# Performance work log

Hardware: AMD Instinct MI355X
Metric: run time of the kernel (lower is better)

The kernel has to match this reference:

```python
import jax, jax.numpy as jnp
import numpy as np
from jax import lax

D_MODEL = 1024
D_STATE = 16
D_CONV = 4
EXPAND = 2
D_INNER = D_MODEL * EXPAND
B, T = 2, 1024


def setup_inputs() -> dict:
    key = jax.random.key(0)
    ks = jax.random.split(key, 8)
    s = 0.02
    x = jax.random.normal(ks[0], (B, T, D_MODEL), dtype=jnp.float32)
    in_proj_w = jax.random.normal(ks[1], (D_MODEL, 2 * D_INNER), dtype=jnp.float32) * s
    conv_w = jax.random.normal(ks[2], (D_INNER, 1, D_CONV), dtype=jnp.float32) * s  # depthwise [O, I/G=1, K]
    conv_b = jax.random.normal(ks[3], (D_INNER,), dtype=jnp.float32) * s
    x_proj_w = jax.random.normal(ks[4], (D_INNER, 2 * D_STATE + 1), dtype=jnp.float32) * s
    dt_proj_w = jax.random.normal(ks[5], (1, D_INNER), dtype=jnp.float32) * s
    dt_proj_b = jax.random.normal(ks[6], (D_INNER,), dtype=jnp.float32) * s
    # Canonical Mamba init: A_log = log(1..d_state) broadcast over d_inner
    A_log = jnp.broadcast_to(jnp.log(jnp.arange(1, D_STATE + 1, dtype=jnp.float32))[None, :], (D_INNER, D_STATE))
    D_param = jnp.ones((D_INNER,), dtype=jnp.float32)
    c_proj_w = jax.random.normal(ks[7], (D_INNER, D_MODEL), dtype=jnp.float32) * s
    return {"x": x, "in_proj_w": in_proj_w, "conv_w": conv_w, "conv_b": conv_b,
            "x_proj_w": x_proj_w, "dt_proj_w": dt_proj_w, "dt_proj_b": dt_proj_b,
            "A_log": A_log, "D_param": D_param, "c_proj_w": c_proj_w}


def _mamba_fwd(x, in_proj_w, conv_w, conv_b, x_proj_w, dt_proj_w, dt_proj_b, A_log, D_param, c_proj_w):
    Bb, Tt, _ = x.shape
    xz = jnp.einsum('btd,de->bte', x, in_proj_w)          # [B,T,2*Di]
    x_branch, z = jnp.split(xz, 2, axis=-1)               # [B,T,Di] each
    # Causal depthwise conv1d: pad left K-1 (== torch pad both + slice[:T])
    xb = jnp.transpose(x_branch, (0, 2, 1))               # [B,Di,T]
    xb = lax.conv_general_dilated(xb, conv_w, window_strides=(1,),
                                  padding=[(D_CONV - 1, 0)],
                                  feature_group_count=D_INNER,
                                  dimension_numbers=('NCH', 'OIH', 'NCH'))
    xb = xb + conv_b[None, :, None]
    x_branch = jax.nn.silu(jnp.transpose(xb, (0, 2, 1)))  # [B,T,Di]
    x_ssm = jnp.einsum('btd,dk->btk', x_branch, x_proj_w) # [B,T,2S+1]
    B_t = x_ssm[:, :, :D_STATE]                            # [B,T,S]
    C_t = x_ssm[:, :, D_STATE:2 * D_STATE]                 # [B,T,S]
    dt = x_ssm[:, :, -1:]                                  # [B,T,1]
    dt = jax.nn.softplus(jnp.einsum('btk,kd->btd', dt, dt_proj_w) + dt_proj_b)  # [B,T,Di]
    A = -jnp.exp(A_log)                                    # [Di,S]
    A_bar = jnp.exp(dt[..., None] * A[None, None])         # [B,T,Di,S]
    Bx = (dt[..., None] * B_t[:, :, None, :]) * x_branch[..., None]  # [B,T,Di,S]

    def step(h, inp):
        a, bx, c = inp                                     # [B,Di,S],[B,Di,S],[B,S]
        h = a * h + bx
        y = jnp.einsum('bds,bs->bd', h, c)
        return h, y

    h0 = jnp.zeros((Bb, D_INNER, D_STATE), dtype=x.dtype)
    _, ys = lax.scan(step, h0,
                     (jnp.transpose(A_bar, (1, 0, 2, 3)),
                      jnp.transpose(Bx, (1, 0, 2, 3)),
                      jnp.transpose(C_t, (1, 0, 2))))
    y = jnp.transpose(ys, (1, 0, 2))                       # [B,T,Di]
    y = y + D_param[None, None, :] * x_branch
    y = y * jax.nn.silu(z)
    return jnp.einsum('btd,de->bte', y, c_proj_w)          # [B,T,d_model]


def reference(x, in_proj_w, conv_w, conv_b, x_proj_w, dt_proj_w, dt_proj_b, A_log, D_param, c_proj_w):
    return _mamba_fwd(x, in_proj_w, conv_w, conv_b, x_proj_w, dt_proj_w, dt_proj_b, A_log, D_param, c_proj_w)
```

## Files before the change

### kernel.cpp

```cpp
#include <hip/hip_runtime.h>
#include <math.h>

#define DMODEL 1024
#define DSTATE 16
#define DCONV 4
#define DINNER 2048
#define BATCH 2
#define SEQ 1024
#define BT (BATCH*SEQ)
#define NC 32
#define LC 32

typedef unsigned short ushort_t;
typedef __attribute__((ext_vector_type(8))) short short8;
typedef __attribute__((ext_vector_type(4))) float f32x4;

__device__ __forceinline__ ushort_t f2bf(float f) {
    union { float f; unsigned int u; } v; v.f = f;
    unsigned int r = v.u + 0x7fffu + ((v.u >> 16) & 1u);
    return (ushort_t)(r >> 16);
}
__device__ __forceinline__ float bf2f(ushort_t u) {
    union { unsigned int u; float f; } v; v.u = ((unsigned int)u) << 16;
    return v.f;
}
__device__ __forceinline__ float softplusf(float x) {
    return (x > 20.f) ? x : log1pf(__expf(x));
}

#define GLOAD_LDS16(G, L) \
  __builtin_amdgcn_global_load_lds((const __attribute__((address_space(1))) void*)(G), \
                                   (__attribute__((address_space(3))) void*)(L), 16, 0, 0)

__global__ __launch_bounds__(256) void prep_kernel(const float* __restrict__ x,
                                                   ushort_t* __restrict__ xbf,
                                                   const float* __restrict__ w1,
                                                   ushort_t* __restrict__ w1T,
                                                   const float* __restrict__ w2,
                                                   ushort_t* __restrict__ w2T,
                                                   float* __restrict__ zacc)
{
    __shared__ float t[32][33];
    const int bid = blockIdx.x;
    const int tid = threadIdx.x;

    if (bid < 1024) {
        size_t i = ((size_t)bid * 256 + tid) * 8;
        float4 a = *(const float4*)&x[i];
        float4 b = *(const float4*)&x[i + 4];
        uint4 p;
        p.x = (unsigned)f2bf(a.x) | ((unsigned)f2bf(a.y) << 16);
        p.y = (unsigned)f2bf(a.z) | ((unsigned)f2bf(a.w) << 16);
        p.z = (unsigned)f2bf(b.x) | ((unsigned)f2bf(b.y) << 16);
        p.w = (unsigned)f2bf(b.z) | ((unsigned)f2bf(b.w) << 16);
        *(uint4*)&xbf[i] = p;
        if (bid < 66) {
            size_t z = ((size_t)bid * 256 + tid) * 4;
            *(float4*)&zacc[z] = make_float4(0.f, 0.f, 0.f, 0.f);
        }
        return;
    }

    const float* in; ushort_t* out; int R, Cc, r0, c0;
    if (bid < 5120) {
        int b2 = bid - 1024;
        in = w1; out = w1T; R = DMODEL; Cc = 2 * DINNER;
        r0 = (b2 >> 7) * 32; c0 = (b2 & 127) * 32;
    } else {
        int b3 = bid - 5120;
        in = w2; out = w2T; R = DINNER; Cc = DMODEL;
        r0 = (b3 >> 5) * 32; c0 = (b3 & 31) * 32;
    }
    {
        int lr = tid >> 3, lc4 = (tid & 7) * 4;
        float4 v = *(const float4*)&in[(size_t)(r0 + lr) * Cc + c0 + lc4];
        t[lr][lc4 + 0] = v.x; t[lr][lc4 + 1] = v.y;
        t[lr][lc4 + 2] = v.z; t[lr][lc4 + 3] = v.w;
    }
    __syncthreads();
    {
        int oc = tid >> 3, rq = (tid & 7) * 4;
        ushort4 u;
        u.x = f2bf(t[rq + 0][oc]);
        u.y = f2bf(t[rq + 1][oc]);
        u.z = f2bf(t[rq + 2][oc]);
        u.w = f2bf(t[rq + 3][oc]);
        *(ushort4*)&out[(size_t)(c0 + oc) * R + r0 + rq] = u;
    }
}

__global__ __launch_bounds__(256) void gemm_in(const ushort_t* __restrict__ A,
                                               const ushort_t* __restrict__ Bt,
                                               float* __restrict__ xzx,
                                               ushort_t* __restrict__ zsil)
{
    constexpr int BM = 128, BN = 128, BK = 64;
    constexpr int AL = BM * BK / (256 * 8);
    constexpr int BL = BN * BK / (256 * 8);
    constexpr int FM = BM / 32;
    constexpr int FN = BN / 32;
    const int K = DMODEL;
    __shared__ __align__(16) ushort_t Al[BM * BK];
    __shared__ __align__(16) ushort_t Bl[BN * BK];

    const int tid  = threadIdx.x;
    const int lane = tid & 63;
    const int wid  = tid >> 6;
    const int wr   = wid >> 1;
    const int wc   = wid & 1;
    const int bm   = blockIdx.y * BM;
    const int bn   = blockIdx.x * BN;

    f32x4 acc[FM][FN] = {};

    for (int k0 = 0; k0 < K; k0 += BK) {
#pragma unroll
        for (int j = 0; j < AL; j++) {
            int chunk = j * 256 + tid;
            GLOAD_LDS16(&A[(size_t)(bm + (chunk >> 3)) * K + k0 + (chunk & 7) * 8],
                        &Al[(size_t)(j * 256 + wid * 64) * 8]);
        }
#pragma unroll
        for (int j = 0; j < BL; j++) {
            int chunk = j * 256 + tid;
            GLOAD_LDS16(&Bt[(size_t)(bn + (chunk >> 3)) * K + k0 + (chunk & 7) * 8],
                        &Bl[(size_t)(j * 256 + wid * 64) * 8]);
        }
        __syncthreads();

#pragma unroll
        for (int kk = 0; kk < 2; kk++) {
            short8 af[FM], bf[FN];
#pragma unroll
            for (int m = 0; m < FM; m++)
                af[m] = *(const short8*)&Al[(wr * (BM / 2) + m * 16 + (lane & 15)) * BK
                                            + (lane >> 4) * 8 + kk * 32];
#pragma unroll
            for (int n = 0; n < FN; n++)
                bf[n] = *(const short8*)&Bl[(wc * (BN / 2) + n * 16 + (lane & 15)) * BK
                                            + (lane >> 4) * 8 + kk * 32];
#pragma unroll
            for (int m = 0; m < FM; m++)
#pragma unroll
                for (int n = 0; n < FN; n++)
                    acc[m][n] = __builtin_amdgcn_mfma_f32_16x16x32_bf16(af[m], bf[n], acc[m][n], 0, 0, 0);
        }
        __syncthreads();
    }

    if (bn < DINNER) {
#pragma unroll
        for (int m = 0; m < FM; m++)
#pragma unroll
            for (int n = 0; n < FN; n++) {
                int row0 = bm + wr * (BM / 2) + m * 16 + (lane >> 4) * 4;
                int col  = bn + wc * (BN / 2) + n * 16 + (lane & 15);
#pragma unroll
                for (int r = 0; r < 4; r++)
                    xzx[(size_t)(row0 + r) * DINNER + col] = acc[m][n][r];
            }
    } else {
#pragma unroll
        for (int m = 0; m < FM; m++)
#pragma unroll
            for (int n = 0; n < FN; n++) {
                int row0 = bm + wr * (BM / 2) + m * 16 + (lane >> 4) * 4;
                int col  = bn - DINNER + wc * (BN / 2) + n * 16 + (lane & 15);
#pragma unroll
                for (int r = 0; r < 4; r++) {
                    float z = acc[m][n][r];
                    zsil[(size_t)(row0 + r) * DINNER + col] = f2bf(z / (1.f + __expf(-z)));
                }
            }
    }
}

template<int BM, int BN>
__global__ __launch_bounds__(256) void gemm_bt(const ushort_t* __restrict__ A,
                                               const ushort_t* __restrict__ Bt,
                                               float* __restrict__ C,
                                               int M, int N, int K)
{
    constexpr int BK = 64;
    constexpr int AL = BM * BK / (256 * 8);
    constexpr int BL = BN * BK / (256 * 8);
    constexpr int FM = BM / 32;
    constexpr int FN = BN / 32;
    __shared__ __align__(16) ushort_t Al[BM * BK];
    __shared__ __align__(16) ushort_t Bl[BN * BK];

    const int tid  = threadIdx.x;
    const int lane = tid & 63;
    const int wid  = tid >> 6;
    const int wr   = wid >> 1;
    const int wc   = wid & 1;
    const int bm   = blockIdx.y * BM;
    const int bn   = blockIdx.x * BN;

    f32x4 acc[FM][FN] = {};

    for (int k0 = 0; k0 < K; k0 += BK) {
#pragma unroll
        for (int j = 0; j < AL; j++) {
            int chunk = j * 256 + tid;
            GLOAD_LDS16(&A[(size_t)(bm + (chunk >> 3)) * K + k0 + (chunk & 7) * 8],
                        &Al[(size_t)(j * 256 + wid * 64) * 8]);
        }
#pragma unroll
        for (int j = 0; j < BL; j++) {
            int chunk = j * 256 + tid;
            GLOAD_LDS16(&Bt[(size_t)(bn + (chunk >> 3)) * K + k0 + (chunk & 7) * 8],
                        &Bl[(size_t)(j * 256 + wid * 64) * 8]);
        }
        __syncthreads();

#pragma unroll
        for (int kk = 0; kk < 2; kk++) {
            short8 af[FM], bf[FN];
#pragma unroll
            for (int m = 0; m < FM; m++)
                af[m] = *(const short8*)&Al[(wr * (BM / 2) + m * 16 + (lane & 15)) * BK
                                            + (lane >> 4) * 8 + kk * 32];
#pragma unroll
            for (int n = 0; n < FN; n++)
                bf[n] = *(const short8*)&Bl[(wc * (BN / 2) + n * 16 + (lane & 15)) * BK
                                            + (lane >> 4) * 8 + kk * 32];
#pragma unroll
            for (int m = 0; m < FM; m++)
#pragma unroll
                for (int n = 0; n < FN; n++)
                    acc[m][n] = __builtin_amdgcn_mfma_f32_16x16x32_bf16(af[m], bf[n], acc[m][n], 0, 0, 0);
        }
        __syncthreads();
    }

#pragma unroll
    for (int m = 0; m < FM; m++)
#pragma unroll
        for (int n = 0; n < FN; n++) {
            int row0 = bm + wr * (BM / 2) + m * 16 + (lane >> 4) * 4;
            int col  = bn + wc * (BN / 2) + n * 16 + (lane & 15);
#pragma unroll
            for (int r = 0; r < 4; r++)
                C[(size_t)(row0 + r) * N + col] = acc[m][n][r];
        }
}

__global__ __launch_bounds__(256) void conv_silu_kernel(const float* __restrict__ xzx,
                                                        const float* __restrict__ cw,
                                                        const float* __restrict__ cb,
                                                        float* __restrict__ xb_rm)
{
    __shared__ float tile[64 + 3][64];
    const int b  = blockIdx.z;
    const int t0 = blockIdx.x * 64;
    const int d0 = blockIdx.y * 64;
    const int tid = threadIdx.x;

    for (int e = tid; e < 67 * 16; e += 256) {
        int r  = e / 16;
        int c4 = (e % 16) * 4;
        int t  = t0 - 3 + r;
        float4 v = make_float4(0.f, 0.f, 0.f, 0.f);
        if (t >= 0)
            v = *(const float4*)&xzx[((size_t)b * SEQ + t) * DINNER + d0 + c4];
        *(float4*)&tile[r][c4] = v;
    }
    __syncthreads();

    const int dl = tid & 63;
    const int tb = tid >> 6;
    const int d  = d0 + dl;
    const float w0 = cw[d * 4 + 0], w1 = cw[d * 4 + 1];
    const float w2 = cw[d * 4 + 2], w3 = cw[d * 4 + 3];
    const float bias = cb[d];

#pragma unroll
    for (int ii = 0; ii < 16; ii++) {
        int tl = tb + 4 * ii;
        float s = bias;
        s = fmaf(tile[tl + 0][dl], w0, s);
        s = fmaf(tile[tl + 1][dl], w1, s);
        s = fmaf(tile[tl + 2][dl], w2, s);
        s = fmaf(tile[tl + 3][dl], w3, s);
        float sil = s / (1.f + __expf(-s));
        xb_rm[((size_t)b * SEQ + t0 + tl) * DINNER + d] = sil;
    }
}

__global__ __launch_bounds__(256) void xproj_kernel(const float* __restrict__ xb,
                                                    const float* __restrict__ w,
                                                    float* __restrict__ Btb,
                                                    float* __restrict__ Ctb,
                                                    float* __restrict__ dtraw)
{
    __shared__ float xs[8][256];
    __shared__ float ws[256][33];
    const int bt0 = blockIdx.x * 8;
    const int kc  = blockIdx.y * 256;
    const int tid = threadIdx.x;
    const int r = tid >> 5, n = tid & 31;

#pragma unroll
    for (int j = 0; j < 2; j++) {
        int e4 = (j * 256 + tid) * 4;
        int rr = e4 >> 8, cc = e4 & 255;
        *(float4*)&xs[rr][cc] = *(const float4*)&xb[(size_t)(bt0 + rr) * DINNER + kc + cc];
    }
    {
        const float* wsrc = w + (size_t)kc * 33;
        float* wdst = &ws[0][0];
        for (int e4 = tid; e4 < 2112; e4 += 256)
            *(float4*)&wdst[e4 * 4] = *(const float4*)&wsrc[e4 * 4];
    }
    __syncthreads();

    float acc = 0.f;
#pragma unroll 16
    for (int kk = 0; kk < 256; kk += 4) {
        float4 xv = *(const float4*)&xs[r][kk];
        acc = fmaf(xv.x, ws[kk + 0][n], acc);
        acc = fmaf(xv.y, ws[kk + 1][n], acc);
        acc = fmaf(xv.z, ws[kk + 2][n], acc);
        acc = fmaf(xv.w, ws[kk + 3][n], acc);
    }
    float dacc = 0.f;
#pragma unroll
    for (int j = 0; j < 8; j++)
        dacc = fmaf(xs[r][n * 8 + j], ws[n * 8 + j][32], dacc);
#pragma unroll
    for (int off = 16; off; off >>= 1)
        dacc += __shfl_xor(dacc, off, 32);

    if (n < 16) atomicAdd(&Btb[(bt0 + r) * 16 + n], acc);
    else        atomicAdd(&Ctb[(bt0 + r) * 16 + (n - 16)], acc);
    if (n == 0) atomicAdd(&dtraw[bt0 + r], dacc);
}

__device__ __forceinline__ void qpowers(float q, float* a)
{
    float q2 = q * q, q4 = q2 * q2, q8 = q4 * q4;
    a[0] = q;        a[1] = q2;       a[2] = q2 * q;   a[3] = q4;
    a[4] = q4 * q;   a[5] = q4 * q2;  a[6] = q4 * a[2];a[7] = q8;
    a[8] = q8 * q;   a[9] = q8 * q2;  a[10]= q8 * a[2];a[11]= q8 * q4;
    a[12]= q8 * a[4];a[13]= q8 * a[5];a[14]= q8 * a[6];a[15]= q8 * q8;
}

__device__ __forceinline__ bool a_structure_ok(const float* A_log, int d, float As2_0)
{
    bool ok = true;
#pragma unroll
    for (int s = 1; s < 16; s++) {
        float v = -__expf(A_log[d * 16 + s]) * 1.44269504f;
        ok &= (fabsf(v - (float)(s + 1) * As2_0) <= 1e-4f * (float)(s + 1) * fabsf(As2_0));
    }
    return ok;
}

__global__ __launch_bounds__(256) void scan1_kernel(const float* __restrict__ xb,
                                                    const float* __restrict__ dtraw,
                                                    const float* __restrict__ Btb,
                                                    const float* __restrict__ A_log,
                                                    const float* __restrict__ dtw,
                                                    const float* __restrict__ dtb,
                                                    float* __restrict__ Hend,
                                                    float* __restrict__ dtsum)
{
    __shared__ float raw[LC];
    __shared__ float xs[LC][256];
    __shared__ float Bs[LC][16];

    const int tid = threadIdx.x;
    const int c   = blockIdx.x;
    const int b   = blockIdx.z;
    const int d0  = blockIdx.y * 256;
    const int d   = d0 + tid;
    const int t0  = c * LC;

    if (tid < LC / 4)
        *(float4*)&raw[tid * 4] = *(const float4*)&dtraw[b * SEQ + t0 + tid * 4];
    if (tid < 128)
        *(float4*)&Bs[0][tid * 4] = *(const float4*)&Btb[((size_t)b * SEQ + t0) * 16 + tid * 4];
#pragma unroll
    for (int j = 0; j < 8; j++) {
        int e = j * 256 + tid;
        int rr = e >> 6, c4 = (e & 63) * 4;
        *(float4*)&xs[rr][c4] = *(const float4*)&xb[((size_t)b * SEQ + t0 + rr) * DINNER + d0 + c4];
    }

    const float wd = dtw[d], bd = dtb[d];
    const float As2_0 = -__expf(A_log[d * 16]) * 1.44269504f;
    const bool fast = a_structure_ok(A_log, d, As2_0);

    float h[16];
#pragma unroll
    for (int s = 0; s < 16; s++) h[s] = 0.f;
    float dsum = 0.f;
    __syncthreads();

    if (fast) {
#pragma unroll 2
        for (int t = 0; t < LC; t++) {
            float dt = softplusf(fmaf(raw[t], wd, bd));
            float xv = xs[t][tid];
            float Bv[16];
#pragma unroll
            for (int s4 = 0; s4 < 4; s4++)
                *(float4*)&Bv[s4 * 4] = *(const float4*)&Bs[t][s4 * 4];
            float a[16];
            qpowers(exp2f(dt * As2_0), a);
            float dtx = dt * xv;
            dsum += dt;
#pragma unroll
            for (int s = 0; s < 16; s++)
                h[s] = fmaf(a[s], h[s], Bv[s] * dtx);
        }
    } else {
        float As2[16];
#pragma unroll
        for (int s = 0; s < 16; s++)
            As2[s] = -__expf(A_log[d * 16 + s]) * 1.44269504f;
#pragma unroll 2
        for (int t = 0; t < LC; t++) {
            float dt = softplusf(fmaf(raw[t], wd, bd));
            float xv = xs[t][tid];
            float Bv[16];
#pragma unroll
            for (int s4 = 0; s4 < 4; s4++)
                *(float4*)&Bv[s4 * 4] = *(const float4*)&Bs[t][s4 * 4];
            float dtx = dt * xv;
            dsum += dt;
#pragma unroll
            for (int s = 0; s < 16; s++)
                h[s] = fmaf(exp2f(dt * As2[s]), h[s], Bv[s] * dtx);
        }
    }

    size_t hb = (((size_t)b * NC + c) * DINNER + d) * 16;
#pragma unroll
    for (int s4 = 0; s4 < 4; s4++)
        *(float4*)&Hend[hb + s4 * 4] = *(float4*)&h[s4 * 4];
    dtsum[((size_t)b * NC + c) * DINNER + d] = dsum;
}

__global__ __launch_bounds__(256) void carry_kernel(const float* __restrict__ Hend,
                                                    const float* __restrict__ dtsum,
                                                    const float* __restrict__ A_log,
                                                    float* __restrict__ Hstart)
{
    const int idx = blockIdx.x * 256 + threadIdx.x;
    const int s = idx & 15;
    const int d = (idx >> 4) & (DINNER - 1);
    const int b = idx >> 15;
    const float As2 = -__expf(A_log[d * 16 + s]) * 1.44269504f;
    float hs = 0.f;
    for (int c = 0; c < NC; c++) {
        size_t off = ((size_t)b * NC + c);
        float P  = exp2f(As2 * dtsum[off * DINNER + d]);
        size_t hi = (off * DINNER + d) * 16 + s;
        float he = Hend[hi];
        Hstart[hi] = hs;
        hs = fmaf(P, hs, he);
    }
}

__global__ __launch_bounds__(256) void scan3_kernel(const float* __restrict__ xb,
                                                    const float* __restrict__ dtraw,
                                                    const float* __restrict__ Btb,
                                                    const float* __restrict__ Ctb,
                                                    const float* __restrict__ A_log,
                                                    const float* __restrict__ dtw,
                                                    const float* __restrict__ dtb,
                                                    const float* __restrict__ Hstart,
                                                    const ushort_t* __restrict__ zsil,
                                                    const float* __restrict__ Dp,
                                                    ushort_t* __restrict__ ygb)
{
    __shared__ float raw[LC];
    __shared__ float xs[LC][256];
    __shared__ float Bs[LC][16];
    __shared__ float Cs[LC][16];

    const int tid = threadIdx.x;
    const int c   = blockIdx.x;
    const int b   = blockIdx.z;
    const int d0  = blockIdx.y * 256;
    const int d   = d0 + tid;
    const int t0  = c * LC;

    if (tid < LC / 4)
        *(float4*)&raw[tid * 4] = *(const float4*)&dtraw[b * SEQ + t0 + tid * 4];
    if (tid < 128)
        *(float4*)&Bs[0][tid * 4] = *(const float4*)&Btb[((size_t)b * SEQ + t0) * 16 + tid * 4];
    else {
        int u = tid - 128;
        *(float4*)&Cs[0][u * 4] = *(const float4*)&Ctb[((size_t)b * SEQ + t0) * 16 + u * 4];
    }
#pragma unroll
    for (int j = 0; j < 8; j++) {
        int e = j * 256 + tid;
        int rr = e >> 6, c4 = (e & 63) * 4;
        *(float4*)&xs[rr][c4] = *(const float4*)&xb[((size_t)b * SEQ + t0 + rr) * DINNER + d0 + c4];
    }

    const float wd = dtw[d], bd = dtb[d];
    const float Dd = Dp[d];
    const float As2_0 = -__expf(A_log[d * 16]) * 1.44269504f;
    const bool fast = a_structure_ok(A_log, d, As2_0);

    float h[16];
    {
        size_t hb = (((size_t)b * NC + c) * DINNER + d) * 16;
#pragma unroll
        for (int s4 = 0; s4 < 4; s4++)
            *(float4*)&h[s4 * 4] = *(const float4*)&Hstart[hb + s4 * 4];
    }
    __syncthreads();

    if (fast) {
#pragma unroll 2
        for (int t = 0; t < LC; t++) {
            float dt = softplusf(fmaf(raw[t], wd, bd));
            float xv = xs[t][tid];
            float Bv[16], Cv[16];
#pragma unroll
            for (int s4 = 0; s4 < 4; s4++) {
                *(float4*)&Bv[s4 * 4] = *(const float4*)&Bs[t][s4 * 4];
                *(float4*)&Cv[s4 * 4] = *(const float4*)&Cs[t][s4 * 4];
            }
            float a[16];
            qpowers(exp2f(dt * As2_0), a);
            float dtx = dt * xv;
            float acc = 0.f;
#pragma unroll
            for (int s = 0; s < 16; s++) {
                h[s] = fmaf(a[s], h[s], Bv[s] * dtx);
                acc = fmaf(h[s], Cv[s], acc);
            }
            xs[t][tid] = fmaf(Dd, xv, acc);
        }
    } else {
        float As2[16];
#pragma unroll
        for (int s = 0; s < 16; s++)
            As2[s] = -__expf(A_log[d * 16 + s]) * 1.44269504f;
#pragma unroll 2
        for (int t = 0; t < LC; t++) {
            float dt = softplusf(fmaf(raw[t], wd, bd));
            float xv = xs[t][tid];
            float Bv[16], Cv[16];
#pragma unroll
            for (int s4 = 0; s4 < 4; s4++) {
                *(float4*)&Bv[s4 * 4] = *(const float4*)&Bs[t][s4 * 4];
                *(float4*)&Cv[s4 * 4] = *(const float4*)&Cs[t][s4 * 4];
            }
            float dtx = dt * xv;
            float acc = 0.f;
#pragma unroll
            for (int s = 0; s < 16; s++) {
                h[s] = fmaf(exp2f(dt * As2[s]), h[s], Bv[s] * dtx);
                acc = fmaf(h[s], Cv[s], acc);
            }
            xs[t][tid] = fmaf(Dd, xv, acc);
        }
    }
    __syncthreads();

#pragma unroll
    for (int j = 0; j < 8; j++) {
        int e = j * 256 + tid;
        int rr = e >> 6, c4 = (e & 63) * 4;
        float4 yv = *(const float4*)&xs[rr][c4];
        ushort4 zv = *(const ushort4*)&zsil[((size_t)b * SEQ + t0 + rr) * DINNER + d0 + c4];
        ushort4 u;
        u.x = f2bf(yv.x * bf2f(zv.x));
        u.y = f2bf(yv.y * bf2f(zv.y));
        u.z = f2bf(yv.z * bf2f(zv.z));
        u.w = f2bf(yv.w * bf2f(zv.w));
        *(ushort4*)&ygb[((size_t)b * SEQ + t0 + rr) * DINNER + d0 + c4] = u;
    }
}

extern "C" void kernel_launch(void* const* d_in, const int* in_sizes, int n_in,
                              void* d_out, int out_size, void* d_ws, size_t ws_size,
                              hipStream_t stream)
{
    const float* x         = (const float*)d_in[0];
    const float* in_proj_w = (const float*)d_in[1];
    const float* conv_w    = (const float*)d_in[2];
    const float* conv_b    = (const float*)d_in[3];
    const float* x_proj_w  = (const float*)d_in[4];
    const float* dt_proj_w = (const float*)d_in[5];
    const float* dt_proj_b = (const float*)d_in[6];
    const float* A_log     = (const float*)d_in[7];
    const float* D_param   = (const float*)d_in[8];
    const float* c_proj_w  = (const float*)d_in[9];
    float* out = (float*)d_out;

    float* ws    = (float*)d_ws;
    float* xzx   = ws;
    float* xb    = xzx + (size_t)BT * DINNER;
    float* Btb   = xb  + (size_t)BT * DINNER;
    float* Ctb   = Btb + (size_t)BT * 16;
    float* dtraw = Ctb + (size_t)BT * 16;
    float* Hend  = dtraw + BT;
    float* Hstart= Hend + (size_t)BATCH * NC * DINNER * 16;
    float* dtsum = Hstart + (size_t)BATCH * NC * DINNER * 16;
    ushort_t* xbf  = (ushort_t*)(dtsum + (size_t)BATCH * NC * DINNER);
    ushort_t* w1T  = xbf + (size_t)BT * DMODEL;
    ushort_t* w2T  = w1T + (size_t)(2 * DINNER) * DMODEL;
    ushort_t* ygb  = w2T + (size_t)DMODEL * DINNER;
    ushort_t* zsil = ygb + (size_t)BT * DINNER;

    prep_kernel<<<dim3(1024 + 4096 + 2048), 256, 0, stream>>>(
        x, xbf, in_proj_w, w1T, c_proj_w, w2T, Btb);

    gemm_in<<<dim3((2 * DINNER) / 128, BT / 128), 256, 0, stream>>>(
        xbf, w1T, xzx, zsil);

    conv_silu_kernel<<<dim3(SEQ / 64, DINNER / 64, BATCH), 256, 0, stream>>>(
        xzx, conv_w, conv_b, xb);

    xproj_kernel<<<dim3(BT / 8, 8), 256, 0, stream>>>(xb, x_proj_w, Btb, Ctb, dtraw);

    scan1_kernel<<<dim3(NC, DINNER / 256, BATCH), 256, 0, stream>>>(
        xb, dtraw, Btb, A_log, dt_proj_w, dt_proj_b, Hend, dtsum);
    carry_kernel<<<dim3(BATCH * DINNER * 16 / 256), 256, 0, stream>>>(
        Hend, dtsum, A_log, Hstart);
    scan3_kernel<<<dim3(NC, DINNER / 256, BATCH), 256, 0, stream>>>(
        xb, dtraw, Btb, Ctb, A_log, dt_proj_w, dt_proj_b, Hstart, zsil, D_param, ygb);

    gemm_bt<64, 64><<<dim3(DMODEL / 64, BT / 64), 256, 0, stream>>>(
        ygb, w2T, out, BT, DMODEL, DINNER);
}
```

Measured before the change: 156.7 us.

## Store conv output in bf16 and fold chunk carry into scan3

The conv+SiLU output is now written as bf16 and read back as bf16 by xproj, scan1 and scan3, halving the traffic for that activation. The separate carry kernel is removed. Each scan3 block instead recomputes its starting state by folding the chunk-end states of all earlier chunks, using the power structure of A on the fast path. This drops one launch and the Hstart buffer, but adds redundant O(c) serial work per block (up to 31 chunk loads of 16 floats each) and a precision loss on the x branch.

```diff
diff --git a/kernel.cpp b/kernel.cpp
--- a/kernel.cpp
+++ b/kernel.cpp
@@ -249,7 +249,7 @@
 __global__ __launch_bounds__(256) void conv_silu_kernel(const float* __restrict__ xzx,
                                                         const float* __restrict__ cw,
                                                         const float* __restrict__ cb,
-                                                        float* __restrict__ xb_rm)
+                                                        ushort_t* __restrict__ xbb)
 {
     __shared__ float tile[64 + 3][64];
     const int b  = blockIdx.z;
@@ -284,11 +284,11 @@
         s = fmaf(tile[tl + 2][dl], w2, s);
         s = fmaf(tile[tl + 3][dl], w3, s);
         float sil = s / (1.f + __expf(-s));
-        xb_rm[((size_t)b * SEQ + t0 + tl) * DINNER + d] = sil;
-    }
-}
-
-__global__ __launch_bounds__(256) void xproj_kernel(const float* __restrict__ xb,
+        xbb[((size_t)b * SEQ + t0 + tl) * DINNER + d] = f2bf(sil);
+    }
+}
+
+__global__ __launch_bounds__(256) void xproj_kernel(const ushort_t* __restrict__ xbb,
                                                     const float* __restrict__ w,
                                                     float* __restrict__ Btb,
                                                     float* __restrict__ Ctb,
@@ -301,11 +301,12 @@
     const int tid = threadIdx.x;
     const int r = tid >> 5, n = tid & 31;
 
-#pragma unroll
-    for (int j = 0; j < 2; j++) {
-        int e4 = (j * 256 + tid) * 4;
-        int rr = e4 >> 8, cc = e4 & 255;
-        *(float4*)&xs[rr][cc] = *(const float4*)&xb[(size_t)(bt0 + rr) * DINNER + kc + cc];
+    {
+        int rr = tid >> 5, cc8 = (tid & 31) * 8;
+        short8 v = *(const short8*)&xbb[(size_t)(bt0 + rr) * DINNER + kc + cc8];
+#pragma unroll
+        for (int k = 0; k < 8; k++)
+            xs[rr][cc8 + k] = bf2f((ushort_t)v[k]);
     }
     {
         const float* wsrc = w + (size_t)kc * 33;
@@ -357,7 +358,22 @@
     return ok;
 }
 
-__global__ __launch_bounds__(256) void scan1_kernel(const float* __restrict__ xb,
+__device__ __forceinline__ void stage_xs(const ushort_t* __restrict__ xbb,
+                                         float (*xs)[256],
+                                         int b, int t0, int d0, int tid)
+{
+#pragma unroll
+    for (int j = 0; j < 4; j++) {
+        int e = j * 256 + tid;
+        int rr = e >> 5, cc8 = (e & 31) * 8;
+        short8 v = *(const short8*)&xbb[((size_t)b * SEQ + t0 + rr) * DINNER + d0 + cc8];
+#pragma unroll
+        for (int k = 0; k < 8; k++)
+            xs[rr][cc8 + k] = bf2f((ushort_t)v[k]);
+    }
+}
+
+__global__ __launch_bounds__(256) void scan1_kernel(const ushort_t* __restrict__ xbb,
                                                     const float* __restrict__ dtraw,
                                                     const float* __restrict__ Btb,
                                                     const float* __restrict__ A_log,
@@ -381,12 +397,7 @@
         *(float4*)&raw[tid * 4] = *(const float4*)&dtraw[b * SEQ + t0 + tid * 4];
     if (tid < 128)
         *(float4*)&Bs[0][tid * 4] = *(const float4*)&Btb[((size_t)b * SEQ + t0) * 16 + tid * 4];
-#pragma unroll
-    for (int j = 0; j < 8; j++) {
-        int e = j * 256 + tid;
-        int rr = e >> 6, c4 = (e & 63) * 4;
-        *(float4*)&xs[rr][c4] = *(const float4*)&xb[((size_t)b * SEQ + t0 + rr) * DINNER + d0 + c4];
-    }
+    stage_xs(xbb, xs, b, t0, d0, tid);
 
     const float wd = dtw[d], bd = dtb[d];
     const float As2_0 = -__expf(A_log[d * 16]) * 1.44269504f;
@@ -443,35 +454,15 @@
     dtsum[((size_t)b * NC + c) * DINNER + d] = dsum;
 }
 
-__global__ __launch_bounds__(256) void carry_kernel(const float* __restrict__ Hend,
-                                                    const float* __restrict__ dtsum,
-                                                    const float* __restrict__ A_log,
-                                                    float* __restrict__ Hstart)
-{
-    const int idx = blockIdx.x * 256 + threadIdx.x;
-    const int s = idx & 15;
-    const int d = (idx >> 4) & (DINNER - 1);
-    const int b = idx >> 15;
-    const float As2 = -__expf(A_log[d * 16 + s]) * 1.44269504f;
-    float hs = 0.f;
-    for (int c = 0; c < NC; c++) {
-        size_t off = ((size_t)b * NC + c);
-        float P  = exp2f(As2 * dtsum[off * DINNER + d]);
-        size_t hi = (off * DINNER + d) * 16 + s;
-        float he = Hend[hi];
-        Hstart[hi] = hs;
-        hs = fmaf(P, hs, he);
-    }
-}
-
-__global__ __launch_bounds__(256) void scan3_kernel(const float* __restrict__ xb,
+__global__ __launch_bounds__(256) void scan3_kernel(const ushort_t* __restrict__ xbb,
                                                     const float* __restrict__ dtraw,
                                                     const float* __restrict__ Btb,
                                                     const float* __restrict__ Ctb,
                                                     const float* __restrict__ A_log,
                                                     const float* __restrict__ dtw,
                                                     const float* __restrict__ dtb,
-                                                    const float* __restrict__ Hstart,
+                                                    const float* __restrict__ Hend,
+                                                    const float* __restrict__ dtsum,
                                                     const ushort_t* __restrict__ zsil,
                                                     const float* __restrict__ Dp,
                                                     ushort_t* __restrict__ ygb)
@@ -496,12 +487,7 @@
         int u = tid - 128;
         *(float4*)&Cs[0][u * 4] = *(const float4*)&Ctb[((size_t)b * SEQ + t0) * 16 + u * 4];
     }
-#pragma unroll
-    for (int j = 0; j < 8; j++) {
-        int e = j * 256 + tid;
-        int rr = e >> 6, c4 = (e & 63) * 4;
-        *(float4*)&xs[rr][c4] = *(const float4*)&xb[((size_t)b * SEQ + t0 + rr) * DINNER + d0 + c4];
-    }
+    stage_xs(xbb, xs, b, t0, d0, tid);
 
     const float wd = dtw[d], bd = dtb[d];
     const float Dd = Dp[d];
@@ -509,11 +495,40 @@
     const bool fast = a_structure_ok(A_log, d, As2_0);
 
     float h[16];
-    {
-        size_t hb = (((size_t)b * NC + c) * DINNER + d) * 16;
-#pragma unroll
-        for (int s4 = 0; s4 < 4; s4++)
-            *(float4*)&h[s4 * 4] = *(const float4*)&Hstart[hb + s4 * 4];
+#pragma unroll
+    for (int s = 0; s < 16; s++) h[s] = 0.f;
+
+    if (fast) {
+        for (int cc = 0; cc < c; cc++) {
+            size_t off = (size_t)b * NC + cc;
+            float P[16];
+            qpowers(exp2f(As2_0 * dtsum[off * DINNER + d]), P);
+            size_t hi = (off * DINNER + d) * 16;
+            float He[16];
+#pragma unroll
+            for (int s4 = 0; s4 < 4; s4++)
+                *(float4*)&He[s4 * 4] = *(const float4*)&Hend[hi + s4 * 4];
+#pragma unroll
+            for (int s = 0; s < 16; s++)
+                h[s] = fmaf(P[s], h[s], He[s]);
+        }
+    } else {
+        float As2[16];
+#pragma unroll
+        for (int s = 0; s < 16; s++)
+            As2[s] = -__expf(A_log[d * 16 + s]) * 1.44269504f;
+        for (int cc = 0; cc < c; cc++) {
+            size_t off = (size_t)b * NC + cc;
+            float ds = dtsum[off * DINNER + d];
+            size_t hi = (off * DINNER + d) * 16;
+            float He[16];
+#pragma unroll
+            for (int s4 = 0; s4 < 4; s4++)
+                *(float4*)&He[s4 * 4] = *(const float4*)&Hend[hi + s4 * 4];
+#pragma unroll
+            for (int s = 0; s < 16; s++)
+                h[s] = fmaf(exp2f(As2[s] * ds), h[s], He[s]);
+        }
     }
     __syncthreads();
 
@@ -599,18 +614,17 @@
 
     float* ws    = (float*)d_ws;
     float* xzx   = ws;
-    float* xb    = xzx + (size_t)BT * DINNER;
-    float* Btb   = xb  + (size_t)BT * DINNER;
+    float* Btb   = xzx + (size_t)BT * DINNER;
     float* Ctb   = Btb + (size_t)BT * 16;
     float* dtraw = Ctb + (size_t)BT * 16;
     float* Hend  = dtraw + BT;
-    float* Hstart= Hend + (size_t)BATCH * NC * DINNER * 16;
-    float* dtsum = Hstart + (size_t)BATCH * NC * DINNER * 16;
+    float* dtsum = Hend + (size_t)BATCH * NC * DINNER * 16;
     ushort_t* xbf  = (ushort_t*)(dtsum + (size_t)BATCH * NC * DINNER);
     ushort_t* w1T  = xbf + (size_t)BT * DMODEL;
     ushort_t* w2T  = w1T + (size_t)(2 * DINNER) * DMODEL;
     ushort_t* ygb  = w2T + (size_t)DMODEL * DINNER;
     ushort_t* zsil = ygb + (size_t)BT * DINNER;
+    ushort_t* xbb  = zsil + (size_t)BT * DINNER;
 
     prep_kernel<<<dim3(1024 + 4096 + 2048), 256, 0, stream>>>(
         x, xbf, in_proj_w, w1T, c_proj_w, w2T, Btb);
@@ -619,16 +633,15 @@
         xbf, w1T, xzx, zsil);
 
     conv_silu_kernel<<<dim3(SEQ / 64, DINNER / 64, BATCH), 256, 0, stream>>>(
-        xzx, conv_w, conv_b, xb);
-
-    xproj_kernel<<<dim3(BT / 8, 8), 256, 0, stream>>>(xb, x_proj_w, Btb, Ctb, dtraw);
+        xzx, conv_w, conv_b, xbb);
+
+    xproj_kernel<<<dim3(BT / 8, 8), 256, 0, stream>>>(xbb, x_proj_w, Btb, Ctb, dtraw);
 
     scan1_kernel<<<dim3(NC, DINNER / 256, BATCH), 256, 0, stream>>>(
-        xb, dtraw, Btb, A_log, dt_proj_w, dt_proj_b, Hend, dtsum);
-    carry_kernel<<<dim3(BATCH * DINNER * 16 / 256), 256, 0, stream>>>(
-        Hend, dtsum, A_log, Hstart);
+        xbb, dtraw, Btb, A_log, dt_proj_w, dt_proj_b, Hend, dtsum);
     scan3_kernel<<<dim3(NC, DINNER / 256, BATCH), 256, 0, stream>>>(
-        xb, dtraw, Btb, Ctb, A_log, dt_proj_w, dt_proj_b, Hstart, zsil, D_param, ygb);
+        xbb, dtraw, Btb, Ctb, A_log, dt_proj_w, dt_proj_b, Hend, dtsum,
+        zsil, D_param, ygb);
 
     gemm_bt<64, 64><<<dim3(DMODEL / 64, BT / 64), 256, 0, stream>>>(
         ygb, w2T, out, BT, DMODEL, DINNER);
```

After: 162.4 us. 1.04x slower.
